# Optimization experiments

Measured on AMD Instinct MI355X. Metric: run time of the kernel, lower is better.

## Reference

```python
import jax, jax.numpy as jnp
import numpy as np

DILATION_RATE = 4
SEGMENT_SIZE = 512


def setup_inputs() -> dict:
    key = jax.random.key(0)
    x = jax.random.normal(key, (4, 8192, 1024), dtype=jnp.float32)
    return {"x": x}


def reference(x):
    """LongNet-style dilated attention.

    For each offset in range(dilation_rate): take the strided slice
    x[:, offset::r, :], split it into segments of length `segment_size`,
    run full softmax(q k^T / sqrt(d)) v attention inside each segment
    (q=k=v=the slice; attention dim is the full d_model, matching how the
    original feeds [B, n_seg, seg, d_model] to FlashAttention), scatter the
    result back to the strided positions, and average the dilation heads
    (softmax over uniform logits == 1/r weights).

    Since seq_len % (r * segment_size) == 0, the r strided slices tile the
    sequence exactly, so we vectorize over offsets with a single reshape:
    position p = i*r + offset  ->  xr[:, i, offset, :].
    """
    r, seg = DILATION_RATE, SEGMENT_SIZE
    B, S, D = x.shape
    n = S // r            # tokens per strided slice
    g = n // seg          # segments per slice
    scale = 1.0 / jnp.sqrt(jnp.asarray(D, dtype=x.dtype))

    xs = x.reshape(B, g, seg, r, D)  # [B, g, seg, r, D]; axis r = dilation offset
    # segment-local attention, independently per (batch, offset, segment)
    scores = jnp.einsum("bgqrd,bgkrd->brgqk", xs, xs) * scale  # [B, r, g, seg, seg]
    probs = jax.nn.softmax(scores, axis=-1)
    out = jnp.einsum("brgqk,bgkrd->bgqrd", probs, xs)          # [B, g, seg, r, D]
    # scatter back to strided positions (pure reshape, since slices tile S),
    # then weighted sum with uniform softmax weights == divide by r.
    return out.reshape(B, S, D) / r
```

## Files before the change

### kernel.cpp

```cpp
#include <hip/hip_runtime.h>
#include <stdint.h>

typedef __bf16 bf16x8  __attribute__((ext_vector_type(8)));
typedef float  f32x4   __attribute__((ext_vector_type(4)));

#define LOG2E    1.44269504088896340736f
#define SM_SCALE 0.03125f

typedef __attribute__((address_space(1))) const uint32_t gau32;
typedef __attribute__((address_space(3))) uint32_t       lau32;
#define GLD16(g, l) __builtin_amdgcn_global_load_lds((gau32*)(g), (lau32*)(l), 16, 0, 0)

__device__ __forceinline__ uint32_t f2bf(float f) {
  uint32_t u = __builtin_bit_cast(uint32_t, f);
  u += 0x7FFFu + ((u >> 16) & 1u);
  return u >> 16;
}
__device__ __forceinline__ uint32_t pk2(float a, float b) {
  return f2bf(a) | (f2bf(b) << 16);
}
__device__ __forceinline__ uint4 pack8(float4 a, float4 b) {
  uint4 r;
  r.x = pk2(a.x, a.y); r.y = pk2(a.z, a.w);
  r.z = pk2(b.x, b.y); r.w = pk2(b.z, b.w);
  return r;
}

__global__ __launch_bounds__(256)
void prep_comb(const float* __restrict__ x, uint16_t* __restrict__ vt,
               uint16_t* __restrict__ xf) {
  __shared__ char tl[64 * 144];
  const int t    = threadIdx.x;
  const int blk  = blockIdx.x;
  const int dc   = blk & 15;
  const int kb   = (blk >> 4) & 7;
  const int prob = blk >> 7;
  const int b  = prob >> 4, off = (prob >> 2) & 3, gs = prob & 3;

  const int key = t >> 2, dq = t & 3;
  const float* src = x + ((size_t)(b * 8192 + gs * 2048 + (kb * 64 + key) * 4 + off)) * 1024
                     + dc * 64 + dq * 16;
  float4 f0 = *(const float4*)(src);
  float4 f1 = *(const float4*)(src + 4);
  float4 f2 = *(const float4*)(src + 8);
  float4 f3 = *(const float4*)(src + 12);
  const int swz = (key & 7) << 4;
  *(uint4*)(tl + key * 144 + ((dq * 32) ^ swz))      = pack8(f0, f1);
  *(uint4*)(tl + key * 144 + ((dq * 32 + 16) ^ swz)) = pack8(f2, f3);
  __syncthreads();
  {
    const int d = t >> 2, kq = t & 3;
    uint32_t w[8];
#pragma unroll
    for (int i = 0; i < 8; ++i) {
      int k0 = kq * 16 + 2 * i, k1 = k0 + 1;
      uint32_t a  = *(const uint16_t*)(tl + k0 * 144 + ((2 * d) ^ ((k0 & 7) << 4)));
      uint32_t bb = *(const uint16_t*)(tl + k1 * 144 + ((2 * d) ^ ((k1 & 7) << 4)));
      w[i] = a | (bb << 16);
    }
    uint16_t* dst = vt + ((size_t)(prob * 1024 + dc * 64 + d)) * 512 + kb * 64 + kq * 16;
    *(uint4*)(dst)     = *(uint4*)&w[0];
    *(uint4*)(dst + 8) = *(uint4*)&w[4];
  }
  {
    const int row = t >> 2, p = t & 3;
    const int dcl = p >> 1;
    const int dq8b = (p & 1) * 2;
    const int swz2 = (row & 7) << 4;
    char* fbase = (char*)xf +
        (((size_t)(prob * 32 + kb * 4 + (row >> 4)) * 32) + (dc * 2 + dcl)) * 1024;
#pragma unroll
    for (int i = 0; i < 2; ++i) {
      const int dq8 = dq8b + i;
      uint4 w = *(const uint4*)(tl + row * 144 + ((dcl * 64 + dq8 * 16) ^ swz2));
      *(uint4*)(fbase + ((row & 15) + 16 * dq8) * 16) = w;
    }
  }
}

#define R9_0 131072
#define R9_1 139264
#define LDS9_BYTES 147456

__global__ __launch_bounds__(1024, 4)
void dilattn9(const char* __restrict__ xf, const char* __restrict__ vt,
              float* __restrict__ out) {
  extern __shared__ char smem[];

  const int tid  = threadIdx.x;
  const int lane = tid & 63;
  const int wid  = tid >> 6;
  const int h    = lane >> 4;
  const int l15  = lane & 15;
  const int lane16 = lane * 16;

  const int blk  = blockIdx.x;
  const int jj   = blk >> 3;
  const int prob = ((blk & 7) << 3) + (jj >> 2);
  const int q0   = (jj & 3) * 128;
  const int b    = prob >> 4;
  const int off  = (prob >> 2) & 3;
  const int gs   = prob & 3;

  const char* xfp = xf + (size_t)prob * 1048576;
  const int qtile0 = q0 >> 4;
  const char* xfA = xfp + (size_t)(2 * wid) * 32768 + lane16;

  f32x4 S[2][8];
#pragma unroll
  for (int i = 0; i < 2; ++i)
#pragma unroll
    for (int j = 0; j < 8; ++j) S[i][j] = (f32x4){0.f, 0.f, 0.f, 0.f};

#pragma unroll 1
  for (int half = 0; half < 2; ++half) {
#pragma unroll
    for (int i = 0; i < 8; ++i) {
      const int c_ = wid * 8 + i;
      const int dcl = c_ >> 3, qt = c_ & 7;
      GLD16(xfp + ((size_t)(qtile0 + qt) * 32 + (half * 16 + dcl)) * 1024 + lane16,
            smem + dcl * 8192 + qt * 1024);
    }
    __syncthreads();
#pragma unroll
    for (int dc = 0; dc < 16; ++dc) {
      const int dca = half * 16 + dc;
      bf16x8 a0 = *(const bf16x8*)(xfA + dca * 1024);
      bf16x8 a1 = *(const bf16x8*)(xfA + 32768 + dca * 1024);
      const char* qb = smem + dc * 8192 + lane16;
      bf16x8 bq[8];
#pragma unroll
      for (int qt = 0; qt < 8; ++qt)
        bq[qt] = *(const bf16x8*)(qb + qt * 1024);
      __builtin_amdgcn_s_setprio(1);
#pragma unroll
      for (int qt = 0; qt < 8; ++qt) {
        S[0][qt] = __builtin_amdgcn_mfma_f32_16x16x32_bf16(a0, bq[qt], S[0][qt], 0, 0, 0);
        S[1][qt] = __builtin_amdgcn_mfma_f32_16x16x32_bf16(a1, bq[qt], S[1][qt], 0, 0, 0);
      }
      __builtin_amdgcn_s_setprio(0);
    }
    __syncthreads();
  }

  float mq[8], sq[8], rinv[8];
#pragma unroll
  for (int qt = 0; qt < 8; ++qt) {
    float m = S[0][qt][0];
#pragma unroll
    for (int kt = 0; kt < 2; ++kt)
#pragma unroll
      for (int r = 0; r < 4; ++r) m = fmaxf(m, S[kt][qt][r]);
    m = fmaxf(m, __shfl_xor(m, 16, 64));
    m = fmaxf(m, __shfl_xor(m, 32, 64));
    mq[qt] = m;
  }
  if (h == 0) {
#pragma unroll
    for (int qt = 0; qt < 8; ++qt)
      *(float*)(smem + R9_0 + (wid * 128 + qt * 16 + l15) * 4) = mq[qt];
  }
  __syncthreads();
#pragma unroll
  for (int qt = 0; qt < 8; ++qt) {
    float m = -3e38f;
#pragma unroll
    for (int w = 0; w < 16; ++w)
      m = fmaxf(m, *(const float*)(smem + R9_0 + (w * 128 + qt * 16 + l15) * 4));
    mq[qt] = m * SM_SCALE;
    sq[qt] = 0.f;
  }
#pragma unroll
  for (int kt = 0; kt < 2; ++kt)
#pragma unroll
    for (int qt = 0; qt < 8; ++qt)
#pragma unroll
      for (int r = 0; r < 4; ++r) {
        float v = exp2f((S[kt][qt][r] * SM_SCALE - mq[qt]) * LOG2E);
        S[kt][qt][r] = v;
        sq[qt] += v;
      }
#pragma unroll
  for (int qt = 0; qt < 8; ++qt) {
    sq[qt] += __shfl_xor(sq[qt], 16, 64);
    sq[qt] += __shfl_xor(sq[qt], 32, 64);
  }
  if (h == 0) {
#pragma unroll
    for (int qt = 0; qt < 8; ++qt)
      *(float*)(smem + R9_1 + (wid * 128 + qt * 16 + l15) * 4) = sq[qt];
  }
  __syncthreads();
#pragma unroll
  for (int qt = 0; qt < 8; ++qt) {
    float l = 0.f;
#pragma unroll
    for (int w = 0; w < 16; ++w)
      l += *(const float*)(smem + R9_1 + (w * 128 + qt * 16 + l15) * 4);
    rinv[qt] = 0.25f / l;
  }
#pragma unroll
  for (int kt = 0; kt < 2; ++kt)
#pragma unroll
    for (int qt = 0; qt < 8; ++qt) {
      uint2 w2;
      w2.x = pk2(S[kt][qt][0] * rinv[qt], S[kt][qt][1] * rinv[qt]);
      w2.y = pk2(S[kt][qt][2] * rinv[qt], S[kt][qt][3] * rinv[qt]);
      *(uint2*)(smem + qt * 16384 + wid * 1024 +
                (l15 + 16 * (2 * kt + (h >> 1))) * 16 + 8 * (h & 1)) = w2;
    }
  __syncthreads();

#pragma unroll 1
  for (int p = 0; p < 2; ++p) {
    const int dbase = p * 512 + 32 * wid;
    f32x4 acc[2][8];
#pragma unroll
    for (int i = 0; i < 2; ++i)
#pragma unroll
      for (int j = 0; j < 8; ++j) acc[i][j] = (f32x4){0.f, 0.f, 0.f, 0.f};

    const char* vtW = vt + (size_t)prob * 1048576 + (size_t)(dbase + l15) * 1024 + 16 * h;
#pragma unroll 1
    for (int ks = 0; ks < 16; ++ks) {
      bf16x8 pa[8];
#pragma unroll
      for (int qt = 0; qt < 8; ++qt)
        pa[qt] = *(const bf16x8*)(smem + qt * 16384 + ks * 1024 + lane16);
      bf16x8 v0 = *(const bf16x8*)(vtW + ks * 64);
      bf16x8 v1 = *(const bf16x8*)(vtW + 16384 + ks * 64);
      __builtin_amdgcn_s_setprio(1);
#pragma unroll
      for (int qt = 0; qt < 8; ++qt) {
        acc[0][qt] = __builtin_amdgcn_mfma_f32_16x16x32_bf16(pa[qt], v0, acc[0][qt], 0, 0, 0);
        acc[1][qt] = __builtin_amdgcn_mfma_f32_16x16x32_bf16(pa[qt], v1, acc[1][qt], 0, 0, 0);
      }
      __builtin_amdgcn_s_setprio(0);
    }
    float* outW = out + ((size_t)(b * 8192 + gs * 2048 + (q0 + 4 * h) * 4 + off)) * 1024
                  + dbase + l15;
#pragma unroll
    for (int cd = 0; cd < 2; ++cd)
#pragma unroll
      for (int qt = 0; qt < 8; ++qt)
#pragma unroll
        for (int r = 0; r < 4; ++r)
          outW[(size_t)((16 * qt + r) * 4) * 1024 + cd * 16] = acc[cd][qt][r];
  }
}

#define KP_OFF 0
#define Q_OFF  65536
#define RED0   65536
#define RED1   67584
#define LDS_BYTES 73728

__global__ __launch_bounds__(256)
void vt_prepass(const float* __restrict__ x, uint16_t* __restrict__ vt) {
  __shared__ char tl[64 * 144];
  const int t    = threadIdx.x;
  const int blk  = blockIdx.x;
  const int dc   = blk & 15;
  const int kb   = (blk >> 4) & 7;
  const int prob = blk >> 7;
  const int b  = prob >> 4, off = (prob >> 2) & 3, gs = prob & 3;

  const int key = t >> 2, dq = t & 3;
  const float* src = x + ((size_t)(b * 8192 + gs * 2048 + (kb * 64 + key) * 4 + off)) * 1024
                     + dc * 64 + dq * 16;
  float4 f0 = *(const float4*)(src);
  float4 f1 = *(const float4*)(src + 4);
  float4 f2 = *(const float4*)(src + 8);
  float4 f3 = *(const float4*)(src + 12);
  const int swz = (key & 7) << 4;
  *(uint4*)(tl + key * 144 + ((dq * 32) ^ swz))      = pack8(f0, f1);
  *(uint4*)(tl + key * 144 + ((dq * 32 + 16) ^ swz)) = pack8(f2, f3);
  __syncthreads();
  const int d = t >> 2, kq = t & 3;
  uint32_t w[8];
#pragma unroll
  for (int i = 0; i < 8; ++i) {
    int k0 = kq * 16 + 2 * i, k1 = k0 + 1;
    uint32_t a  = *(const uint16_t*)(tl + k0 * 144 + ((2 * d) ^ ((k0 & 7) << 4)));
    uint32_t bb = *(const uint16_t*)(tl + k1 * 144 + ((2 * d) ^ ((k1 & 7) << 4)));
    w[i] = a | (bb << 16);
  }
  uint16_t* dst = vt + ((size_t)(prob * 1024 + dc * 64 + d)) * 512 + kb * 64 + kq * 16;
  *(uint4*)(dst)     = *(uint4*)&w[0];
  *(uint4*)(dst + 8) = *(uint4*)&w[4];
}

template <int USE_VT>
__global__ __launch_bounds__(512, 2)
void dilattn2(const float* __restrict__ x, const uint16_t* __restrict__ vt,
              float* __restrict__ out) {
  extern __shared__ char smem[];

  const int tid  = threadIdx.x;
  const int lane = tid & 63;
  const int wid  = tid >> 6;
  const int h    = lane >> 4;
  const int l15  = lane & 15;
  const int psw  = (l15 & 7) << 4;

  const int blk  = blockIdx.x;
  const int prob = blk >> 3;
  const int q0   = (blk & 7) * 64;
  const int b    = prob >> 4;
  const int off  = (prob >> 2) & 3;
  const int gs   = prob & 3;

  const float* xb = x + (size_t)b * (8192u * 1024u);

  const int srow = tid >> 3;
  const int sg   = tid & 7;
  const float* gK = xb + (size_t)(gs * 2048 + srow * 4 + off) * 1024 + sg * 8;
  const float* gQ = xb + (size_t)(gs * 2048 + (q0 + srow) * 4 + off) * 1024 + sg * 8;
  const int kWr = srow * 128 + ((sg * 16) ^ ((srow & 7) << 4));
  const int qWr = Q_OFF + kWr;

  const int akR = (64 * wid + l15) * 128;
  const int bqR = Q_OFF + l15 * 128;
  const int fb0 = (16 * h) ^ psw;

  f32x4 S[4][4];
#pragma unroll
  for (int i = 0; i < 4; ++i)
#pragma unroll
    for (int j = 0; j < 4; ++j) S[i][j] = (f32x4){0.f, 0.f, 0.f, 0.f};

  float4 kp[16], qp[2];
#pragma unroll
  for (int j = 0; j < 8; ++j) {
    const float* p = gK + (size_t)j * 262144;
    kp[2 * j]     = *(const float4*)(p);
    kp[2 * j + 1] = *(const float4*)(p + 4);
  }
  qp[0] = *(const float4*)(gQ);
  qp[1] = *(const float4*)(gQ + 4);

#pragma unroll 1
  for (int dc = 0; dc < 16; ++dc) {
#pragma unroll
    for (int j = 0; j < 8; ++j)
      *(uint4*)(smem + KP_OFF + kWr + j * 8192) = pack8(kp[2 * j], kp[2 * j + 1]);
    *(uint4*)(smem + qWr) = pack8(qp[0], qp[1]);
    if (dc < 15) {
      const int doff = (dc + 1) * 64;
#pragma unroll
      for (int j = 0; j < 8; ++j) {
        const float* p = gK + (size_t)j * 262144 + doff;
        kp[2 * j]     = *(const float4*)(p);
        kp[2 * j + 1] = *(const float4*)(p + 4);
      }
      qp[0] = *(const float4*)(gQ + doff);
      qp[1] = *(const float4*)(gQ + doff + 4);
    }
    __syncthreads();
#pragma unroll
    for (int s = 0; s < 2; ++s) {
      const int fb = fb0 ^ (s << 6);
      bf16x8 aK[4], bq[4];
#pragma unroll
      for (int kt = 0; kt < 4; ++kt)
        aK[kt] = *(const bf16x8*)(smem + akR + kt * 2048 + fb);
#pragma unroll
      for (int qt = 0; qt < 4; ++qt)
        bq[qt] = *(const bf16x8*)(smem + bqR + qt * 2048 + fb);
#pragma unroll
      for (int kt = 0; kt < 4; ++kt)
#pragma unroll
        for (int qt = 0; qt < 4; ++qt)
          S[kt][qt] = __builtin_amdgcn_mfma_f32_16x16x32_bf16(aK[kt], bq[qt], S[kt][qt], 0, 0, 0);
    }
    __syncthreads();
  }

  float mq[4], sq[4], rinv[4];
#pragma unroll
  for (int qt = 0; qt < 4; ++qt) {
    float m = S[0][qt][0];
#pragma unroll
    for (int kt = 0; kt < 4; ++kt)
#pragma unroll
      for (int r = 0; r < 4; ++r) m = fmaxf(m, S[kt][qt][r]);
    m = fmaxf(m, __shfl_xor(m, 16, 64));
    m = fmaxf(m, __shfl_xor(m, 32, 64));
    mq[qt] = m;
  }
  if (h == 0) {
#pragma unroll
    for (int qt = 0; qt < 4; ++qt)
      *(float*)(smem + RED0 + (wid * 64 + 16 * qt + l15) * 4) = mq[qt];
  }
  __syncthreads();
#pragma unroll
  for (int qt = 0; qt < 4; ++qt) {
    float m = -3e38f;
#pragma unroll
    for (int w = 0; w < 8; ++w)
      m = fmaxf(m, *(const float*)(smem + RED0 + (w * 64 + 16 * qt + l15) * 4));
    mq[qt] = m * SM_SCALE;
    sq[qt] = 0.f;
  }
#pragma unroll
  for (int kt = 0; kt < 4; ++kt)
#pragma unroll
    for (int qt = 0; qt < 4; ++qt)
#pragma unroll
      for (int r = 0; r < 4; ++r) {
        float v = exp2f((S[kt][qt][r] * SM_SCALE - mq[qt]) * LOG2E);
        S[kt][qt][r] = v;
        sq[qt] += v;
      }
#pragma unroll
  for (int qt = 0; qt < 4; ++qt) {
    sq[qt] += __shfl_xor(sq[qt], 16, 64);
    sq[qt] += __shfl_xor(sq[qt], 32, 64);
  }
  if (h == 0) {
#pragma unroll
    for (int qt = 0; qt < 4; ++qt)
      *(float*)(smem + RED1 + (wid * 64 + 16 * qt + l15) * 4) = sq[qt];
  }
  __syncthreads();
#pragma unroll
  for (int qt = 0; qt < 4; ++qt) {
    float l = 0.f;
#pragma unroll
    for (int w = 0; w < 8; ++w)
      l += *(const float*)(smem + RED1 + (w * 64 + 16 * qt + l15) * 4);
    rinv[qt] = 0.25f / l;
  }
#pragma unroll
  for (int kt = 0; kt < 4; ++kt)
#pragma unroll
    for (int qt = 0; qt < 4; ++qt) {
      uint2 w2;
      w2.x = pk2(S[kt][qt][0] * rinv[qt], S[kt][qt][1] * rinv[qt]);
      w2.y = pk2(S[kt][qt][2] * rinv[qt], S[kt][qt][3] * rinv[qt]);
      *(uint2*)(smem + KP_OFF + (16 * qt + l15) * 1024 +
                ((128 * wid + 32 * kt + 8 * h) ^ psw)) = w2;
    }
  __syncthreads();

  f32x4 acc[8][4];
#pragma unroll
  for (int i = 0; i < 8; ++i)
#pragma unroll
    for (int j = 0; j < 4; ++j) acc[i][j] = (f32x4){0.f, 0.f, 0.f, 0.f};

  const uint16_t* vtW = nullptr;
  if constexpr (USE_VT)
    vtW = vt + ((size_t)(prob * 1024 + 128 * wid + l15)) * 512 + 8 * h;

#pragma unroll 1
  for (int ks = 0; ks < 16; ++ks) {
    bf16x8 pa[4];
#pragma unroll
    for (int qt = 0; qt < 4; ++qt)
      pa[qt] = *(const bf16x8*)(smem + KP_OFF + (16 * qt + l15) * 1024 +
                                ((64 * ks + 16 * h) ^ psw));
#pragma unroll
    for (int cd = 0; cd < 8; ++cd) {
      bf16x8 v;
      if constexpr (USE_VT) {
        v = *(const bf16x8*)(vtW + (size_t)((cd >> 2) * 64 + (cd & 3) * 16) * 512 + 32 * ks);
      } else {
        const int d = 128 * wid + (cd >> 2) * 64 + (cd & 3) * 16 + l15;
        union { bf16x8 v; uint16_t u[8]; } a0;
#pragma unroll
        for (int jj = 0; jj < 8; ++jj) {
          int key = 32 * ks + 8 * h + jj;
          a0.u[jj] = (uint16_t)f2bf(xb[(size_t)(gs * 2048 + key * 4 + off) * 1024 + d]);
        }
        v = a0.v;
      }
#pragma unroll
      for (int qt = 0; qt < 4; ++qt)
        acc[cd][qt] = __builtin_amdgcn_mfma_f32_16x16x32_bf16(pa[qt], v, acc[cd][qt], 0, 0, 0);
    }
  }

#pragma unroll
  for (int cd = 0; cd < 8; ++cd) {
    const int d = 128 * wid + (cd >> 2) * 64 + (cd & 3) * 16 + l15;
#pragma unroll
    for (int qt = 0; qt < 4; ++qt)
#pragma unroll
      for (int r = 0; r < 4; ++r) {
        const int qq = q0 + 16 * qt + 4 * h + r;
        out[((size_t)(b * 8192 + gs * 2048 + qq * 4 + off)) * 1024 + d] = acc[cd][qt][r];
      }
  }
}

extern "C" void kernel_launch(void* const* d_in, const int* in_sizes, int n_in,
                              void* d_out, int out_size, void* d_ws, size_t ws_size,
                              hipStream_t stream) {
  const float* x = (const float*)d_in[0];
  float* out = (float*)d_out;
  (void)in_sizes; (void)n_in; (void)out_size;
  const size_t vt_bytes = 64ull * 1024 * 512 * 2;
  const size_t xf_bytes = 64ull * 1024 * 1024;
  if (ws_size >= vt_bytes + xf_bytes) {
    uint16_t* vtp = (uint16_t*)d_ws;
    uint16_t* xfp = (uint16_t*)((char*)d_ws + vt_bytes);
    hipFuncSetAttribute(reinterpret_cast<const void*>(dilattn9),
                        hipFuncAttributeMaxDynamicSharedMemorySize, LDS9_BYTES);
    prep_comb<<<8192, 256, 0, stream>>>(x, vtp, xfp);
    dilattn9<<<256, 1024, LDS9_BYTES, stream>>>((const char*)xfp, (const char*)vtp, out);
  } else if (ws_size >= vt_bytes) {
    uint16_t* vtp = (uint16_t*)d_ws;
    hipFuncSetAttribute(reinterpret_cast<const void*>(dilattn2<1>),
                        hipFuncAttributeMaxDynamicSharedMemorySize, LDS_BYTES);
    vt_prepass<<<8192, 256, 0, stream>>>(x, vtp);
    dilattn2<1><<<512, 512, LDS_BYTES, stream>>>(x, vtp, out);
  } else {
    hipFuncSetAttribute(reinterpret_cast<const void*>(dilattn2<0>),
                        hipFuncAttributeMaxDynamicSharedMemorySize, LDS_BYTES);
    dilattn2<0><<<512, 512, LDS_BYTES, stream>>>(x, nullptr, out);
  }
}
```

Before: 172.6 us.

## Double-buffer K operand loads through LDS ring and prefetch V in PV loop

After: 170.9 us. About the same (-1.0%).

```diff
diff --git a/kernel.cpp b/kernel.cpp
--- a/kernel.cpp
+++ b/kernel.cpp
@@ -10,6 +10,10 @@
 typedef __attribute__((address_space(1))) const uint32_t gau32;
 typedef __attribute__((address_space(3))) uint32_t       lau32;
 #define GLD16(g, l) __builtin_amdgcn_global_load_lds((gau32*)(g), (lau32*)(l), 16, 0, 0)
+#define VMW2() asm volatile("s_waitcnt vmcnt(2)" ::: "memory")
+#define VMW0() asm volatile("s_waitcnt vmcnt(0)" ::: "memory")
+#define LGKM_BAR() do { asm volatile("s_waitcnt lgkmcnt(0)" ::: "memory"); \
+  __builtin_amdgcn_s_barrier(); asm volatile("" ::: "memory"); } while (0)
 
 __device__ __forceinline__ uint32_t f2bf(float f) {
   uint32_t u = __builtin_bit_cast(uint32_t, f);
@@ -78,13 +82,13 @@
   }
 }
 
-#define R9_0 131072
-#define R9_1 139264
-#define LDS9_BYTES 147456
+#define RA_0 131072
+#define RA_1 139264
+#define LDSA_BYTES 147456
 
 __global__ __launch_bounds__(1024, 4)
-void dilattn9(const char* __restrict__ xf, const char* __restrict__ vt,
-              float* __restrict__ out) {
+void dilattn10(const char* __restrict__ xf, const char* __restrict__ vt,
+               float* __restrict__ out) {
   extern __shared__ char smem[];
 
   const int tid  = threadIdx.x;
@@ -105,6 +109,11 @@
   const char* xfp = xf + (size_t)prob * 1048576;
   const int qtile0 = q0 >> 4;
   const char* xfA = xfp + (size_t)(2 * wid) * 32768 + lane16;
+  char* ring = smem + 65536 + wid * 4096;
+
+#define ISSUE_A10(dca, s) do {                                                    \
+    GLD16(xfA + (dca) * 1024, ring + (s) * 2048);                                 \
+    GLD16(xfA + 32768 + (dca) * 1024, ring + (s) * 2048 + 1024); } while (0)
 
   f32x4 S[2][8];
 #pragma unroll
@@ -113,20 +122,25 @@
     for (int j = 0; j < 8; ++j) S[i][j] = (f32x4){0.f, 0.f, 0.f, 0.f};
 
 #pragma unroll 1
-  for (int half = 0; half < 2; ++half) {
-#pragma unroll
-    for (int i = 0; i < 8; ++i) {
-      const int c_ = wid * 8 + i;
+  for (int quarter = 0; quarter < 4; ++quarter) {
+#pragma unroll
+    for (int i = 0; i < 4; ++i) {
+      const int c_ = wid * 4 + i;
       const int dcl = c_ >> 3, qt = c_ & 7;
-      GLD16(xfp + ((size_t)(qtile0 + qt) * 32 + (half * 16 + dcl)) * 1024 + lane16,
+      GLD16(xfp + ((size_t)(qtile0 + qt) * 32 + (quarter * 8 + dcl)) * 1024 + lane16,
             smem + dcl * 8192 + qt * 1024);
     }
-    __syncthreads();
-#pragma unroll
-    for (int dc = 0; dc < 16; ++dc) {
-      const int dca = half * 16 + dc;
-      bf16x8 a0 = *(const bf16x8*)(xfA + dca * 1024);
-      bf16x8 a1 = *(const bf16x8*)(xfA + 32768 + dca * 1024);
+    ISSUE_A10(quarter * 8 + 0, 0);
+    ISSUE_A10(quarter * 8 + 1, 1);
+    VMW2();
+    __builtin_amdgcn_s_barrier();
+    asm volatile("" ::: "memory");
+#pragma unroll
+    for (int dc = 0; dc < 8; ++dc) {
+      if (dc >= 1) { if (dc < 7) VMW2(); else VMW0(); }
+      const char* av = ring + (dc & 1) * 2048 + lane16;
+      bf16x8 a0 = *(const bf16x8*)(av);
+      bf16x8 a1 = *(const bf16x8*)(av + 1024);
       const char* qb = smem + dc * 8192 + lane16;
       bf16x8 bq[8];
 #pragma unroll
@@ -139,8 +153,9 @@
         S[1][qt] = __builtin_amdgcn_mfma_f32_16x16x32_bf16(a1, bq[qt], S[1][qt], 0, 0, 0);
       }
       __builtin_amdgcn_s_setprio(0);
-    }
-    __syncthreads();
+      if (dc < 6) ISSUE_A10(quarter * 8 + dc + 2, dc & 1);
+    }
+    LGKM_BAR();
   }
 
   float mq[8], sq[8], rinv[8];
@@ -158,7 +173,7 @@
   if (h == 0) {
 #pragma unroll
     for (int qt = 0; qt < 8; ++qt)
-      *(float*)(smem + R9_0 + (wid * 128 + qt * 16 + l15) * 4) = mq[qt];
+      *(float*)(smem + RA_0 + (wid * 128 + qt * 16 + l15) * 4) = mq[qt];
   }
   __syncthreads();
 #pragma unroll
@@ -166,7 +181,7 @@
     float m = -3e38f;
 #pragma unroll
     for (int w = 0; w < 16; ++w)
-      m = fmaxf(m, *(const float*)(smem + R9_0 + (w * 128 + qt * 16 + l15) * 4));
+      m = fmaxf(m, *(const float*)(smem + RA_0 + (w * 128 + qt * 16 + l15) * 4));
     mq[qt] = m * SM_SCALE;
     sq[qt] = 0.f;
   }
@@ -188,7 +203,7 @@
   if (h == 0) {
 #pragma unroll
     for (int qt = 0; qt < 8; ++qt)
-      *(float*)(smem + R9_1 + (wid * 128 + qt * 16 + l15) * 4) = sq[qt];
+      *(float*)(smem + RA_1 + (wid * 128 + qt * 16 + l15) * 4) = sq[qt];
   }
   __syncthreads();
 #pragma unroll
@@ -196,7 +211,7 @@
     float l = 0.f;
 #pragma unroll
     for (int w = 0; w < 16; ++w)
-      l += *(const float*)(smem + R9_1 + (w * 128 + qt * 16 + l15) * 4);
+      l += *(const float*)(smem + RA_1 + (w * 128 + qt * 16 + l15) * 4);
     rinv[qt] = 0.25f / l;
   }
 #pragma unroll
@@ -221,21 +236,27 @@
       for (int j = 0; j < 8; ++j) acc[i][j] = (f32x4){0.f, 0.f, 0.f, 0.f};
 
     const char* vtW = vt + (size_t)prob * 1048576 + (size_t)(dbase + l15) * 1024 + 16 * h;
+    bf16x8 vc0 = *(const bf16x8*)(vtW);
+    bf16x8 vc1 = *(const bf16x8*)(vtW + 16384);
 #pragma unroll 1
     for (int ks = 0; ks < 16; ++ks) {
-      bf16x8 pa[8];
-#pragma unroll
-      for (int qt = 0; qt < 8; ++qt)
-        pa[qt] = *(const bf16x8*)(smem + qt * 16384 + ks * 1024 + lane16);
-      bf16x8 v0 = *(const bf16x8*)(vtW + ks * 64);
-      bf16x8 v1 = *(const bf16x8*)(vtW + 16384 + ks * 64);
+      bf16x8 vn0, vn1;
+      if (ks < 15) {
+        vn0 = *(const bf16x8*)(vtW + (ks + 1) * 64);
+        vn1 = *(const bf16x8*)(vtW + 16384 + (ks + 1) * 64);
+      }
       __builtin_amdgcn_s_setprio(1);
 #pragma unroll
-      for (int qt = 0; qt < 8; ++qt) {
-        acc[0][qt] = __builtin_amdgcn_mfma_f32_16x16x32_bf16(pa[qt], v0, acc[0][qt], 0, 0, 0);
-        acc[1][qt] = __builtin_amdgcn_mfma_f32_16x16x32_bf16(pa[qt], v1, acc[1][qt], 0, 0, 0);
+      for (int qp = 0; qp < 4; ++qp) {
+        bf16x8 pa0 = *(const bf16x8*)(smem + (2 * qp) * 16384 + ks * 1024 + lane16);
+        bf16x8 pa1 = *(const bf16x8*)(smem + (2 * qp + 1) * 16384 + ks * 1024 + lane16);
+        acc[0][2 * qp]     = __builtin_amdgcn_mfma_f32_16x16x32_bf16(pa0, vc0, acc[0][2 * qp], 0, 0, 0);
+        acc[1][2 * qp]     = __builtin_amdgcn_mfma_f32_16x16x32_bf16(pa0, vc1, acc[1][2 * qp], 0, 0, 0);
+        acc[0][2 * qp + 1] = __builtin_amdgcn_mfma_f32_16x16x32_bf16(pa1, vc0, acc[0][2 * qp + 1], 0, 0, 0);
+        acc[1][2 * qp + 1] = __builtin_amdgcn_mfma_f32_16x16x32_bf16(pa1, vc1, acc[1][2 * qp + 1], 0, 0, 0);
       }
       __builtin_amdgcn_s_setprio(0);
+      if (ks < 15) { vc0 = vn0; vc1 = vn1; }
     }
     float* outW = out + ((size_t)(b * 8192 + gs * 2048 + (q0 + 4 * h) * 4 + off)) * 1024
                   + dbase + l15;
@@ -247,6 +268,7 @@
         for (int r = 0; r < 4; ++r)
           outW[(size_t)((16 * qt + r) * 4) * 1024 + cd * 16] = acc[cd][qt][r];
   }
+#undef ISSUE_A10
 }
 
 #define KP_OFF 0
@@ -506,10 +528,10 @@
   if (ws_size >= vt_bytes + xf_bytes) {
     uint16_t* vtp = (uint16_t*)d_ws;
     uint16_t* xfp = (uint16_t*)((char*)d_ws + vt_bytes);
-    hipFuncSetAttribute(reinterpret_cast<const void*>(dilattn9),
-                        hipFuncAttributeMaxDynamicSharedMemorySize, LDS9_BYTES);
+    hipFuncSetAttribute(reinterpret_cast<const void*>(dilattn10),
+                        hipFuncAttributeMaxDynamicSharedMemorySize, LDSA_BYTES);
     prep_comb<<<8192, 256, 0, stream>>>(x, vtp, xfp);
-    dilattn9<<<256, 1024, LDS9_BYTES, stream>>>((const char*)xfp, (const char*)vtp, out);
+    dilattn10<<<256, 1024, LDSA_BYTES, stream>>>((const char*)xfp, (const char*)vtp, out);
   } else if (ws_size >= vt_bytes) {
     uint16_t* vtp = (uint16_t*)d_ws;
     hipFuncSetAttribute(reinterpret_cast<const void*>(dilattn2<1>),
```
